# Kernel optimization log

Hardware: AMD Instinct MI355X
Metric: run time of the kernel (lower is better)

The kernel has to match this reference:

```python
import jax, jax.numpy as jnp
import numpy as np

B, IN, H = 8192, 2048, 2048


def setup_inputs() -> dict:
    key = jax.random.key(0)
    ks = jax.random.split(key, 8)
    inp = {
        "x_t": jax.random.normal(ks[0], (B, IN), dtype=jnp.float32),
        "h_prev": jax.random.normal(ks[1], (B, H), dtype=jnp.float32),
        "W_z": jax.random.normal(ks[2], (IN, H), dtype=jnp.float32) * 0.1,
        "W_r": jax.random.normal(ks[3], (IN, H), dtype=jnp.float32) * 0.1,
        "W_h": jax.random.normal(ks[4], (IN, H), dtype=jnp.float32) * 0.1,
        "U_z": jax.random.normal(ks[5], (H, H), dtype=jnp.float32) * 0.1,
        "U_r": jax.random.normal(ks[6], (H, H), dtype=jnp.float32) * 0.1,
        "U_h": jax.random.normal(ks[7], (H, H), dtype=jnp.float32) * 0.1,
        "b_z": jnp.zeros((H,), dtype=jnp.float32),
        "b_r": jnp.zeros((H,), dtype=jnp.float32),
        "b_h": jnp.zeros((H,), dtype=jnp.float32),
    }
    return inp


def reference(x_t, h_prev, W_z, W_r, W_h, U_z, U_r, U_h, b_z, b_r, b_h):
    # Batch the three input-side GEMMs and the two non-gated hidden-side GEMMs.
    Wx = x_t @ jnp.concatenate([W_z, W_r, W_h], axis=1)          # [B, 3H]
    Uh = h_prev @ jnp.concatenate([U_z, U_r], axis=1)            # [B, 2H]
    H_ = h_prev.shape[1]
    z_t = jax.nn.sigmoid(Wx[:, :H_] + Uh[:, :H_] + b_z)
    r_t = jax.nn.sigmoid(Wx[:, H_:2 * H_] + Uh[:, H_:] + b_r)
    # torch line `r_t * h_prev @ U_h` == (r_t * h_prev) @ U_h (left-to-right)
    h_tilda = jnp.tanh(Wx[:, 2 * H_:] + (r_t * h_prev) @ U_h + b_h)
    h_t = (1.0 - z_t) * h_prev + z_t * h_tilda
    return h_t
```

## Files before the change

### kernel.cpp

```cpp
#include <hip/hip_runtime.h>
#include <cstdint>
#include <cstddef>

#define B_DIM  8192
#define H_DIM  2048
#define LDA    6144
#define LDB    4096
#define NKT    64

typedef __attribute__((ext_vector_type(8))) short  short8;
typedef __attribute__((ext_vector_type(4))) float  float4v;

__device__ __forceinline__ unsigned short f2bf(float f) {
    union { float f; unsigned u; } v; v.f = f;
    unsigned r = v.u + 0x7fffu + ((v.u >> 16) & 1u);
    return (unsigned short)(r >> 16);
}

__device__ __forceinline__ float sigmoidf_(float x) {
    return 1.0f / (1.0f + __expf(-x));
}

#define AS1CV(p) ((const __attribute__((address_space(1))) void*)(p))
#define AS3V(p)  ((__attribute__((address_space(3))) void*)(p))

__global__ void cvt_rows(const float* __restrict__ x, const float* __restrict__ h,
                         unsigned short* __restrict__ Abuf) {
    const float* s = blockIdx.z ? h : x;
    const int coff = blockIdx.z ? 0 : 2048;
    const int row = blockIdx.x;
    const int c = threadIdx.x * 8;
    float4 a = *(const float4*)(s + (size_t)row * 2048 + c);
    float4 b = *(const float4*)(s + (size_t)row * 2048 + c + 4);
    union { unsigned short us[8]; uint4 u4; } o;
    o.us[0] = f2bf(a.x); o.us[1] = f2bf(a.y); o.us[2] = f2bf(a.z); o.us[3] = f2bf(a.w);
    o.us[4] = f2bf(b.x); o.us[5] = f2bf(b.y); o.us[6] = f2bf(b.z); o.us[7] = f2bf(b.w);
    *(uint4*)(Abuf + (size_t)row * LDA + coff + c) = o.u4;
}

struct P6 { const float* s[6]; unsigned short* d[6]; };

__global__ void transpose_cvt(P6 io) {
    __shared__ float tile[64][65];
    const float* src = io.s[blockIdx.z];
    unsigned short* dst = io.d[blockIdx.z];
    const int n0 = blockIdx.x * 64;
    const int k0 = blockIdx.y * 64;
    const int t = threadIdx.x;
#pragma unroll
    for (int p = 0; p < 4; ++p) {
        const int k = p * 16 + (t >> 4);
        const int n4 = (t & 15) * 4;
        float4 v = *(const float4*)(src + (size_t)(k0 + k) * 2048 + n0 + n4);
        tile[n4 + 0][k] = v.x; tile[n4 + 1][k] = v.y;
        tile[n4 + 2][k] = v.z; tile[n4 + 3][k] = v.w;
    }
    __syncthreads();
#pragma unroll
    for (int p = 0; p < 2; ++p) {
        const int n = p * 32 + (t >> 3);
        const int k8 = (t & 7) * 8;
        union { unsigned short us[8]; uint4 u4; } o;
#pragma unroll
        for (int q = 0; q < 8; ++q) o.us[q] = f2bf(tile[n][k8 + q]);
        *(uint4*)(dst + (size_t)(n0 + n) * LDB + k0 + k8) = o.u4;
    }
}

struct Core8Ctx {
    const unsigned short* pA;
    const unsigned short* pB;
    char* lds;
    int t, aoff, wmb, wnb;
};

__device__ __forceinline__ void stage_item(const Core8Ctx& c, int item) {
    int tile = item >> 2;
    if (tile >= NKT) tile = 0;
    const int isB = item & 1;
    const int kh  = (item >> 1) & 1;
    const int sb  = tile & 1;
    const unsigned short* src = (isB ? c.pB : c.pA) + tile * 64 + kh * 32;
    const size_t rstep = (size_t)128 * (isB ? LDB : LDA);
    char* dst = c.lds + sb * 65536 + isB * 32768 + kh * 16384 + c.t * 16;
    __builtin_amdgcn_global_load_lds(AS1CV(src),         AS3V(dst),        16, 0, 0);
    __builtin_amdgcn_global_load_lds(AS1CV(src + rstep), AS3V(dst + 8192), 16, 0, 0);
}

template<int BUF, int KK, int MH, bool LOADB>
__device__ __forceinline__ void phase_t(const Core8Ctx& c, int item,
                                        short8 (&bf)[4], float4v (&acc)[8][4]) {
    short8 af[4];
    const char* ab = c.lds + (BUF * 65536 + KK * 16384) + c.wmb + c.aoff;
#pragma unroll
    for (int i = 0; i < 4; ++i)
        af[i] = *(const short8*)(ab + (MH * 4 + i) * 1024);
    if (LOADB) {
        const char* bb = c.lds + (BUF * 65536 + 32768 + KK * 16384) + c.wnb + c.aoff;
#pragma unroll
        for (int j = 0; j < 4; ++j)
            bf[j] = *(const short8*)(bb + j * 1024);
    }
    stage_item(c, item);
    __builtin_amdgcn_s_barrier();
    __builtin_amdgcn_s_setprio(1);
#pragma unroll
    for (int i = 0; i < 4; ++i)
#pragma unroll
        for (int j = 0; j < 4; ++j)
            acc[MH * 4 + i][j] = __builtin_amdgcn_mfma_f32_16x16x32_bf16(
                af[i], bf[j], acc[MH * 4 + i][j], 0, 0, 0);
    __builtin_amdgcn_s_setprio(0);
}

#define GATE()  asm volatile("s_waitcnt vmcnt(8)" ::: "memory")
#define FENCE() asm volatile("" ::: "memory")
#define BAR()   __builtin_amdgcn_s_barrier()

__device__ __forceinline__ void gemm_core8(const unsigned short* __restrict__ Ag,
                                           const unsigned short* __restrict__ Bg,
                                           int m0, int n0, char* lds,
                                           float4v (&acc)[8][4]) {
    const int t    = threadIdx.x;
    const int lane = t & 63;
    const int wid  = t >> 6;
    Core8Ctx c;
    c.lds = lds; c.t = t;
    c.wmb = (wid >> 2) * 8192;
    c.wnb = (wid & 3) * 4096;
    const int fr  = lane & 15;
    const int seg = lane >> 4;
    c.aoff = (fr >> 1) * 128 + (((((fr & 1) << 2) | seg)) ^ ((fr >> 1) & 7)) * 16;
    const int sS   = (t & 7) ^ ((t >> 3) & 7);
    const int rowS = 2 * (t >> 3) + (sS >> 2);
    const int colS = (sS & 3) * 8;
    c.pA = Ag + (size_t)(m0 + rowS) * LDA + colS;
    c.pB = Bg + (size_t)(n0 + rowS) * LDB + colS;

#pragma unroll
    for (int n = 0; n < 6; ++n) stage_item(c, n);
    GATE(); BAR();

    short8 bf[4];
    for (int it = 0; it < NKT / 2; ++it) {
        const int s0 = 8 * it + 6;
        phase_t<0, 0, 0, true >(c, s0 + 0, bf, acc); FENCE(); BAR();
        phase_t<0, 0, 1, false>(c, s0 + 1, bf, acc); GATE();  BAR();
        phase_t<0, 1, 0, true >(c, s0 + 2, bf, acc); FENCE(); BAR();
        phase_t<0, 1, 1, false>(c, s0 + 3, bf, acc); GATE();  BAR();
        phase_t<1, 0, 0, true >(c, s0 + 4, bf, acc); FENCE(); BAR();
        phase_t<1, 0, 1, false>(c, s0 + 5, bf, acc); GATE();  BAR();
        phase_t<1, 1, 0, true >(c, s0 + 6, bf, acc); FENCE(); BAR();
        phase_t<1, 1, 1, false>(c, s0 + 7, bf, acc); GATE();  BAR();
    }
}

__global__ __launch_bounds__(512, 2) void gemm_zr(const unsigned short* __restrict__ Abuf,
                                                  const unsigned short* __restrict__ Bzr,
                                                  const float* __restrict__ hprev,
                                                  const float* __restrict__ bz,
                                                  const float* __restrict__ br,
                                                  float* __restrict__ zout,
                                                  unsigned short* __restrict__ Arh) {
    extern __shared__ char lds[];
    float4v acc[8][4];
#pragma unroll
    for (int i = 0; i < 8; ++i)
#pragma unroll
        for (int j = 0; j < 4; ++j)
            acc[i][j] = (float4v){0.f, 0.f, 0.f, 0.f};

    int id = blockIdx.x;
    id = (id & 7) * (512 / 8) + (id >> 3);
    const int bm = id % 32, bn = id / 32;
    const int m0 = bm * 256;
    const int n0 = bn * 256;

    gemm_core8(Abuf, Bzr, m0, n0, lds, acc);

    const int t = threadIdx.x, lane = t & 63;
    const int wm = (t >> 6) >> 2, wn = (t >> 6) & 3;
    const int col = lane & 15, rbase = (lane >> 4) * 4;
    const bool zhalf = n0 < 2048;
#pragma unroll
    for (int i = 0; i < 8; ++i)
#pragma unroll
        for (int j = 0; j < 4; ++j) {
            const int gn = n0 + wn * 64 + j * 16 + col;
            const int gm0 = m0 + wm * 128 + i * 16 + rbase;
            if (zhalf) {
                const float bias = bz[gn];
#pragma unroll
                for (int r = 0; r < 4; ++r) {
                    const size_t idx = (size_t)(gm0 + r) * H_DIM + gn;
                    zout[idx] = sigmoidf_(acc[i][j][r] + bias);
                }
            } else {
                const int gn2 = gn - 2048;
                const float bias = br[gn2];
#pragma unroll
                for (int r = 0; r < 4; ++r) {
                    const size_t idx = (size_t)(gm0 + r) * H_DIM + gn2;
                    const float rt = sigmoidf_(acc[i][j][r] + bias);
                    Arh[(size_t)(gm0 + r) * LDA + gn2] = f2bf(rt * hprev[idx]);
                }
            }
        }
}

__global__ __launch_bounds__(512, 2) void gemm_h(const unsigned short* __restrict__ Axrh,
                                                 const unsigned short* __restrict__ Bh,
                                                 const float* __restrict__ hprev,
                                                 const float* __restrict__ bh,
                                                 float* __restrict__ out) {
    extern __shared__ char lds[];
    float4v acc[8][4];
#pragma unroll
    for (int i = 0; i < 8; ++i)
#pragma unroll
        for (int j = 0; j < 4; ++j)
            acc[i][j] = (float4v){0.f, 0.f, 0.f, 0.f};

    int id = blockIdx.x;
    id = (id & 7) * (256 / 8) + (id >> 3);
    const int bm = id % 32, bn = id / 32;
    const int m0 = bm * 256;
    const int n0 = bn * 256;

    gemm_core8(Axrh, Bh, m0, n0, lds, acc);

    const int t = threadIdx.x, lane = t & 63;
    const int wm = (t >> 6) >> 2, wn = (t >> 6) & 3;
    const int col = lane & 15, rbase = (lane >> 4) * 4;
#pragma unroll
    for (int i = 0; i < 8; ++i)
#pragma unroll
        for (int j = 0; j < 4; ++j) {
            const int gn = n0 + wn * 64 + j * 16 + col;
            const int gm0 = m0 + wm * 128 + i * 16 + rbase;
            const float bias = bh[gn];
#pragma unroll
            for (int r = 0; r < 4; ++r) {
                const size_t idx = (size_t)(gm0 + r) * H_DIM + gn;
                const float ht = tanhf(acc[i][j][r] + bias);
                const float z = out[idx];
                const float h = hprev[idx];
                out[idx] = (1.0f - z) * h + z * ht;
            }
        }
}

extern "C" void kernel_launch(void* const* d_in, const int* in_sizes, int n_in,
                              void* d_out, int out_size, void* d_ws, size_t ws_size,
                              hipStream_t stream) {
    const float* x  = (const float*)d_in[0];
    const float* h  = (const float*)d_in[1];
    const float* Wz = (const float*)d_in[2];
    const float* Wr = (const float*)d_in[3];
    const float* Wh = (const float*)d_in[4];
    const float* Uz = (const float*)d_in[5];
    const float* Ur = (const float*)d_in[6];
    const float* Uh = (const float*)d_in[7];
    const float* bz = (const float*)d_in[8];
    const float* br = (const float*)d_in[9];
    const float* bh = (const float*)d_in[10];
    float* out = (float*)d_out;

    char* ws = (char*)d_ws;
    unsigned short* Abuf = (unsigned short*)(ws);
    unsigned short* Bzr  = (unsigned short*)(ws + (size_t)96  * 1024 * 1024);
    unsigned short* Bh   = (unsigned short*)(ws + (size_t)128 * 1024 * 1024);

    (void)hipFuncSetAttribute((const void*)gemm_zr,
                              hipFuncAttributeMaxDynamicSharedMemorySize, 131072);
    (void)hipFuncSetAttribute((const void*)gemm_h,
                              hipFuncAttributeMaxDynamicSharedMemorySize, 131072);

    cvt_rows<<<dim3(B_DIM, 1, 2), 256, 0, stream>>>(x, h, Abuf);

    P6 io;
    io.s[0] = Uz; io.d[0] = Bzr;
    io.s[1] = Wz; io.d[1] = Bzr + 2048;
    io.s[2] = Ur; io.d[2] = Bzr + (size_t)2048 * LDB;
    io.s[3] = Wr; io.d[3] = Bzr + (size_t)2048 * LDB + 2048;
    io.s[4] = Wh; io.d[4] = Bh;
    io.s[5] = Uh; io.d[5] = Bh + 2048;
    transpose_cvt<<<dim3(32, 32, 6), 256, 0, stream>>>(io);

    gemm_zr<<<dim3(512), dim3(512), 131072, stream>>>(Abuf, Bzr, h, bz, br, out,
                                                      Abuf + 4096 );

    gemm_h<<<dim3(256), dim3(512), 131072, stream>>>(Abuf + 2048 ,
                                                     Bh, h, bh, out);
}
```

Before: 730.5 us.

## Double-buffer LDS fragments across phases and remap blocks per XCD

The GEMM inner loop now prefetches the next phase's A/B fragments from LDS into a second register set while the current phase's MFMAs run. This lets each phase use a single barrier with a vmcnt(6) wait instead of a barrier before and after. Block-to-tile mapping in both kernels is also changed so that each XCD works on a compact group of M/N tiles, aimed at better L2 reuse. In exchange it uses more VGPRs for the duplicate fragments, and the new barrier placement could expose LDS hazards if the wait counts are wrong.

```diff
diff --git a/kernel.cpp b/kernel.cpp
--- a/kernel.cpp
+++ b/kernel.cpp
@@ -87,35 +87,35 @@
     __builtin_amdgcn_global_load_lds(AS1CV(src + rstep), AS3V(dst + 8192), 16, 0, 0);
 }
 
-template<int BUF, int KK, int MH, bool LOADB>
-__device__ __forceinline__ void phase_t(const Core8Ctx& c, int item,
-                                        short8 (&bf)[4], float4v (&acc)[8][4]) {
-    short8 af[4];
-    const char* ab = c.lds + (BUF * 65536 + KK * 16384) + c.wmb + c.aoff;
-#pragma unroll
-    for (int i = 0; i < 4; ++i)
-        af[i] = *(const short8*)(ab + (MH * 4 + i) * 1024);
-    if (LOADB) {
-        const char* bb = c.lds + (BUF * 65536 + 32768 + KK * 16384) + c.wnb + c.aoff;
-#pragma unroll
-        for (int j = 0; j < 4; ++j)
-            bf[j] = *(const short8*)(bb + j * 1024);
-    }
+template<int MH, int NBUF, int NKK, int NMH>
+__device__ __forceinline__ void phase2(const Core8Ctx& c, int item,
+                                       short8 (&afc)[4], short8 (&afn)[4],
+                                       short8 (&bfc)[4], short8 (&bfn)[4],
+                                       float4v (&acc)[8][4]) {
     stage_item(c, item);
-    __builtin_amdgcn_s_barrier();
+    {
+        const char* abn = c.lds + (NBUF * 65536 + NKK * 16384) + c.wmb + c.aoff;
+#pragma unroll
+        for (int i = 0; i < 4; ++i)
+            afn[i] = *(const short8*)(abn + (NMH * 4 + i) * 1024);
+        if constexpr (NMH == 0) {
+            const char* bbn = c.lds + (NBUF * 65536 + 32768 + NKK * 16384) + c.wnb + c.aoff;
+#pragma unroll
+            for (int j = 0; j < 4; ++j)
+                bfn[j] = *(const short8*)(bbn + j * 1024);
+        }
+    }
     __builtin_amdgcn_s_setprio(1);
 #pragma unroll
     for (int i = 0; i < 4; ++i)
 #pragma unroll
         for (int j = 0; j < 4; ++j)
             acc[MH * 4 + i][j] = __builtin_amdgcn_mfma_f32_16x16x32_bf16(
-                af[i], bf[j], acc[MH * 4 + i][j], 0, 0, 0);
+                afc[i], bfc[j], acc[MH * 4 + i][j], 0, 0, 0);
     __builtin_amdgcn_s_setprio(0);
-}
-
-#define GATE()  asm volatile("s_waitcnt vmcnt(8)" ::: "memory")
-#define FENCE() asm volatile("" ::: "memory")
-#define BAR()   __builtin_amdgcn_s_barrier()
+    asm volatile("s_waitcnt vmcnt(6)" ::: "memory");
+    __builtin_amdgcn_s_barrier();
+}
 
 __device__ __forceinline__ void gemm_core8(const unsigned short* __restrict__ Ag,
                                            const unsigned short* __restrict__ Bg,
@@ -139,19 +139,29 @@
 
 #pragma unroll
     for (int n = 0; n < 6; ++n) stage_item(c, n);
-    GATE(); BAR();
-
-    short8 bf[4];
+    asm volatile("s_waitcnt vmcnt(8)" ::: "memory");
+    __builtin_amdgcn_s_barrier();
+
+    short8 afA[4], afB[4], bfA[4], bfB[4];
+    {
+        const char* ab = c.lds + c.wmb + c.aoff;
+#pragma unroll
+        for (int i = 0; i < 4; ++i) afA[i] = *(const short8*)(ab + i * 1024);
+        const char* bb = c.lds + 32768 + c.wnb + c.aoff;
+#pragma unroll
+        for (int j = 0; j < 4; ++j) bfA[j] = *(const short8*)(bb + j * 1024);
+    }
+
     for (int it = 0; it < NKT / 2; ++it) {
         const int s0 = 8 * it + 6;
-        phase_t<0, 0, 0, true >(c, s0 + 0, bf, acc); FENCE(); BAR();
-        phase_t<0, 0, 1, false>(c, s0 + 1, bf, acc); GATE();  BAR();
-        phase_t<0, 1, 0, true >(c, s0 + 2, bf, acc); FENCE(); BAR();
-        phase_t<0, 1, 1, false>(c, s0 + 3, bf, acc); GATE();  BAR();
-        phase_t<1, 0, 0, true >(c, s0 + 4, bf, acc); FENCE(); BAR();
-        phase_t<1, 0, 1, false>(c, s0 + 5, bf, acc); GATE();  BAR();
-        phase_t<1, 1, 0, true >(c, s0 + 6, bf, acc); FENCE(); BAR();
-        phase_t<1, 1, 1, false>(c, s0 + 7, bf, acc); GATE();  BAR();
+        phase2<0, 0, 0, 1>(c, s0 + 0, afA, afB, bfA, bfB, acc);
+        phase2<1, 0, 1, 0>(c, s0 + 1, afB, afA, bfA, bfB, acc);
+        phase2<0, 0, 1, 1>(c, s0 + 2, afA, afB, bfB, bfA, acc);
+        phase2<1, 1, 0, 0>(c, s0 + 3, afB, afA, bfB, bfA, acc);
+        phase2<0, 1, 0, 1>(c, s0 + 4, afA, afB, bfA, bfB, acc);
+        phase2<1, 1, 1, 0>(c, s0 + 5, afB, afA, bfA, bfB, acc);
+        phase2<0, 1, 1, 1>(c, s0 + 6, afA, afB, bfB, bfA, acc);
+        phase2<1, 0, 0, 0>(c, s0 + 7, afB, afA, bfB, bfA, acc);
     }
 }
 
@@ -170,9 +180,13 @@
         for (int j = 0; j < 4; ++j)
             acc[i][j] = (float4v){0.f, 0.f, 0.f, 0.f};
 
-    int id = blockIdx.x;
-    id = (id & 7) * (512 / 8) + (id >> 3);
-    const int bm = id % 32, bn = id / 32;
+    const int bid = blockIdx.x;
+    const int x  = bid & 7;
+    const int s  = bid >> 3;
+    const int st = s >> 5;
+    const int w  = s & 31;
+    const int bm = (x >> 1) * 8 + st * 4 + (w & 3);
+    const int bn = (x & 1) * 8 + (w >> 2);
     const int m0 = bm * 256;
     const int n0 = bn * 256;
 
@@ -221,9 +235,10 @@
         for (int j = 0; j < 4; ++j)
             acc[i][j] = (float4v){0.f, 0.f, 0.f, 0.f};
 
-    int id = blockIdx.x;
-    id = (id & 7) * (256 / 8) + (id >> 3);
-    const int bm = id % 32, bn = id / 32;
+    const int bid = blockIdx.x;
+    const int x = bid & 7, s = bid >> 3;
+    const int bm = x * 4 + (s & 3);
+    const int bn = s >> 2;
     const int m0 = bm * 256;
     const int n0 = bn * 256;
 
```

Result: no change. 733.4 us (+0.4%).
